# Performance work log

Measured on AMD Instinct MI355X. Metric: run time of the kernel, lower is better.

## Reference

```python
import jax, jax.numpy as jnp
import numpy as np

N_NODES = 100000
N_EDGES = 3200000
IN_CH = 256


def setup_inputs() -> dict:
    key = jax.random.key(0)
    k1, k2, k3 = jax.random.split(key, 3)
    x = jax.random.normal(k1, (N_NODES, IN_CH), dtype=jnp.float32)
    edge_index = jax.random.randint(k2, (2, N_EDGES), 0, N_NODES, dtype=jnp.int64)
    # GCNConv linear: weight [in_channels, 1] (applied as x @ W), bias [1]
    W = jax.random.normal(k3, (IN_CH, 1), dtype=jnp.float32) * (1.0 / np.sqrt(IN_CH))
    b = jnp.zeros((1,), dtype=jnp.float32)
    return {"x": x, "edge_index": edge_index, "W": W, "b": b}


def reference(x, edge_index, W, b):
    # PyG GCNConv(in, 1): h = x @ W; add self-loops; symmetric norm; scatter-add to target; + bias
    N = x.shape[0]
    self_loops = jnp.broadcast_to(jnp.arange(N, dtype=edge_index.dtype)[None, :], (2, N))
    ei = jnp.concatenate([edge_index, self_loops], axis=1)  # [2, E+N]
    src, dst = ei[0], ei[1]

    # degree computed at target (col) with unit edge weights, incl. self-loops
    deg = jax.ops.segment_sum(jnp.ones(ei.shape[1], dtype=x.dtype), dst, num_segments=N)
    deg_inv_sqrt = jnp.where(deg > 0, jax.lax.rsqrt(deg), 0.0)
    norm = deg_inv_sqrt[src] * deg_inv_sqrt[dst]  # [E+N]

    h = x @ W  # [N, 1] — project first (out_channels < in_channels)
    msg = norm[:, None] * h[src]  # [E+N, 1]
    out = jax.ops.segment_sum(msg, dst, num_segments=N)  # [N, 1]
    return out + b
```

## Files before the change

### kernel.cpp

```cpp
#include <hip/hip_runtime.h>

#define GCN_N 100000
#define GCN_E 3200000
#define GCN_C 256
#define BSHIFT 8
#define NBUCK 391
#define BCAP 9216

#define NPROJ 1024
#define NBIN 512
#define TB 512
#define CHUNK (GCN_E / NBIN)
#define EPT ((CHUNK + TB - 1) / TB)

__global__ void k_init(int* __restrict__ cursor) {
    const int i = threadIdx.x;
    if (i < NBUCK) cursor[i] = 0;
}

__global__ void __launch_bounds__(TB) k_proj_bin(const float* __restrict__ x,
                                                 const float* __restrict__ W,
                                                 float* __restrict__ h,
                                                 const int* __restrict__ src,
                                                 const int* __restrict__ dst,
                                                 int* __restrict__ cursor,
                                                 int* __restrict__ bpack) {
    __shared__ int hist[NBUCK];
    __shared__ int lscan[NBUCK];
    __shared__ int gbase[NBUCK];
    __shared__ int wsum[8], woff[8];
    __shared__ int spack[CHUNK];
    __shared__ int sdest[CHUNK];
    const int tid = threadIdx.x;

    if (blockIdx.x < NPROJ) {
        const int lane   = tid & 63;
        const int wave   = (blockIdx.x * TB + tid) >> 6;
        const int nw4    = NPROJ * (TB / 64) * 4;
        const float4 wf = *reinterpret_cast<const float4*>(W + lane * 4);
        for (int i = wave * 4; i < GCN_N; i += nw4) {
            const float4 a0 = *reinterpret_cast<const float4*>(x + (size_t)(i + 0) * GCN_C + lane * 4);
            const float4 a1 = *reinterpret_cast<const float4*>(x + (size_t)(i + 1) * GCN_C + lane * 4);
            const float4 a2 = *reinterpret_cast<const float4*>(x + (size_t)(i + 2) * GCN_C + lane * 4);
            const float4 a3 = *reinterpret_cast<const float4*>(x + (size_t)(i + 3) * GCN_C + lane * 4);
            float s0 = a0.x * wf.x + a0.y * wf.y + a0.z * wf.z + a0.w * wf.w;
            float s1 = a1.x * wf.x + a1.y * wf.y + a1.z * wf.z + a1.w * wf.w;
            float s2 = a2.x * wf.x + a2.y * wf.y + a2.z * wf.z + a2.w * wf.w;
            float s3 = a3.x * wf.x + a3.y * wf.y + a3.z * wf.z + a3.w * wf.w;
            #pragma unroll
            for (int off = 32; off > 0; off >>= 1) {
                s0 += __shfl_down(s0, off, 64);
                s1 += __shfl_down(s1, off, 64);
                s2 += __shfl_down(s2, off, 64);
                s3 += __shfl_down(s3, off, 64);
            }
            if (lane == 0) { h[i] = s0; h[i + 1] = s1; h[i + 2] = s2; h[i + 3] = s3; }
        }
        return;
    }

    const int blk = blockIdx.x - NPROJ;
    for (int b = tid; b < NBUCK; b += TB) hist[b] = 0;
    __syncthreads();

    const int c0 = blk * CHUNK;
    int my_pack[EPT], my_b[EPT], my_off[EPT];
    #pragma unroll
    for (int j = 0; j < EPT; ++j) {
        const int k = tid + j * TB;
        my_b[j] = -1;
        if (k < CHUNK) {
            const int d = dst[c0 + k];
            const int s = src[c0 + k];
            const int b = d >> BSHIFT;
            my_pack[j] = (s << BSHIFT) | (d & 255);
            my_b[j]    = b;
            my_off[j]  = atomicAdd(&hist[b], 1);
        }
    }
    __syncthreads();

    if (tid < NBUCK) gbase[tid] = atomicAdd(&cursor[tid], hist[tid]);
    {
        const int lane = tid & 63, w = tid >> 6;
        const int v = (tid < NBUCK) ? hist[tid] : 0;
        int incl = v;
        #pragma unroll
        for (int d2 = 1; d2 < 64; d2 <<= 1) {
            const int t = __shfl_up(incl, d2, 64);
            if (lane >= d2) incl += t;
        }
        if (lane == 63) wsum[w] = incl;
        __syncthreads();
        if (tid == 0) { int s = 0; for (int k2 = 0; k2 < 8; ++k2) { woff[k2] = s; s += wsum[k2]; } }
        __syncthreads();
        if (tid < NBUCK) lscan[tid] = incl - v + woff[w];
    }
    __syncthreads();

    #pragma unroll
    for (int j = 0; j < EPT; ++j) {
        if (my_b[j] >= 0) {
            const int b    = my_b[j];
            const int slot = lscan[b] + my_off[j];
            const int goff = gbase[b] + my_off[j];
            spack[slot] = my_pack[j];
            sdest[slot] = (goff < BCAP) ? (b * BCAP + goff) : -1;
        }
    }
    __syncthreads();

    for (int i = tid; i < CHUNK; i += TB) {
        const int dpos = sdest[i];
        if (dpos >= 0) bpack[dpos] = spack[i];
    }
}

__global__ void __launch_bounds__(1024) k_deg_norm(const int* __restrict__ bpack,
                                                   const int* __restrict__ cursor,
                                                   const float* __restrict__ h,
                                                   float* __restrict__ dis,
                                                   float* __restrict__ g) {
    __shared__ int cnt[256];
    const int p = blockIdx.x, tid = threadIdx.x;
    if (tid < 256) cnt[tid] = 0;
    __syncthreads();
    const int s0 = p * BCAP, s1 = s0 + min(cursor[p], BCAP);
    for (int i = s0 + tid; i < s1; i += 1024)
        atomicAdd(&cnt[bpack[i] & 255], 1);
    __syncthreads();
    if (tid < 256) {
        const int node = (p << BSHIFT) + tid;
        if (node < GCN_N) {
            const float r = rsqrtf(1.0f + (float)cnt[tid]);
            dis[node] = r;
            g[node]   = r * h[node];
        }
    }
}

__global__ void __launch_bounds__(1024) k_scatter_bin(const int* __restrict__ bpack,
                                                      const int* __restrict__ cursor,
                                                      const float* __restrict__ g,
                                                      const float* __restrict__ dis,
                                                      const float* __restrict__ bias,
                                                      float* __restrict__ out) {
    __shared__ float acc[256];
    const int p = blockIdx.x, tid = threadIdx.x;
    if (tid < 256) acc[tid] = 0.0f;
    __syncthreads();
    const int s0 = p * BCAP, s1 = s0 + min(cursor[p], BCAP);
    for (int i = s0 + tid; i < s1; i += 1024) {
        const int pk = bpack[i];
        atomicAdd(&acc[pk & 255], g[pk >> BSHIFT]);
    }
    __syncthreads();
    if (tid < 256) {
        const int node = (p << BSHIFT) + tid;
        if (node < GCN_N)
            out[node] = bias[0] + dis[node] * (acc[tid] + g[node]);
    }
}

__global__ void k_zero(float* __restrict__ a, int n) {
    int i = blockIdx.x * blockDim.x + threadIdx.x;
    const int stride = gridDim.x * blockDim.x;
    for (; i < n; i += stride) a[i] = 0.0f;
}
__global__ void k_proj_sep(const float* __restrict__ x, const float* __restrict__ W,
                           float* __restrict__ h, int n) {
    const int lane   = threadIdx.x & 63;
    const int wave   = (blockIdx.x * blockDim.x + threadIdx.x) >> 6;
    const int nwaves = (gridDim.x * blockDim.x) >> 6;
    const float4 wf = *reinterpret_cast<const float4*>(W + lane * 4);
    for (int i = wave; i < n; i += nwaves) {
        const float4 xv = *reinterpret_cast<const float4*>(x + (size_t)i * GCN_C + lane * 4);
        float s = xv.x * wf.x + xv.y * wf.y + xv.z * wf.z + xv.w * wf.w;
        #pragma unroll
        for (int off = 32; off > 0; off >>= 1)
            s += __shfl_down(s, off, 64);
        if (lane == 0) h[i] = s;
    }
}
__global__ void k_degree_flat(const int* __restrict__ dst, float* __restrict__ deg, int e) {
    int i = blockIdx.x * blockDim.x + threadIdx.x;
    const int stride = gridDim.x * blockDim.x;
    for (; i < e; i += stride) atomicAdd(&deg[dst[i]], 1.0f);
}
__global__ void k_norm_flat(const float* __restrict__ h, float* __restrict__ deg_dis,
                            float* __restrict__ out, const float* __restrict__ bias, int n) {
    const int i = blockIdx.x * blockDim.x + threadIdx.x;
    if (i < n) {
        const float r = rsqrtf(deg_dis[i] + 1.0f);
        deg_dis[i] = r;
        out[i] = bias[0] + r * r * h[i];
    }
}
__global__ void k_scatter_flat(const int* __restrict__ src, const int* __restrict__ dst,
                               const float* __restrict__ h, const float* __restrict__ dis,
                               float* __restrict__ out, int e) {
    int i = blockIdx.x * blockDim.x + threadIdx.x;
    const int stride = gridDim.x * blockDim.x;
    for (; i < e; i += stride) {
        const int s = src[i], d = dst[i];
        atomicAdd(&out[d], dis[s] * dis[d] * h[s]);
    }
}

extern "C" void kernel_launch(void* const* d_in, const int* in_sizes, int n_in,
                              void* d_out, int out_size, void* d_ws, size_t ws_size,
                              hipStream_t stream) {
    const float* x  = (const float*)d_in[0];
    const int*   ei = (const int*)d_in[1];
    const float* W  = (const float*)d_in[2];
    const float* b  = (const float*)d_in[3];
    float* out = (float*)d_out;
    const int* src = ei;
    const int* dst = ei + GCN_E;

    float* h      = (float*)d_ws;
    float* dis    = h + GCN_N;
    float* g      = dis + GCN_N;
    int*   cursor = (int*)(g + GCN_N);
    int*   bpack  = cursor + NBUCK;
    const size_t need = ((size_t)3 * GCN_N + NBUCK + (size_t)NBUCK * BCAP) * 4;

    if (ws_size >= need) {
        k_init<<<1, TB, 0, stream>>>(cursor);
        k_proj_bin<<<NPROJ + NBIN, TB, 0, stream>>>(x, W, h, src, dst, cursor, bpack);
        k_deg_norm<<<NBUCK, 1024, 0, stream>>>(bpack, cursor, h, dis, g);
        k_scatter_bin<<<NBUCK, 1024, 0, stream>>>(bpack, cursor, g, dis, b, out);
    } else {
        float* hh  = (float*)d_ws;
        float* deg = hh + GCN_N;
        k_zero<<<512, 256, 0, stream>>>(deg, GCN_N);
        k_proj_sep<<<2048, 256, 0, stream>>>(x, W, hh, GCN_N);
        k_degree_flat<<<2048, 256, 0, stream>>>(dst, deg, GCN_E);
        k_norm_flat<<<(GCN_N + 255) / 256, 256, 0, stream>>>(hh, deg, out, b, GCN_N);
        k_scatter_flat<<<2048, 256, 0, stream>>>(src, dst, hh, deg, out, GCN_E);
    }
}
```

Before: 72.18 us.

## Fuse projection into binning blocks instead of separate projection blocks

Removes the dedicated projection blocks and has each of 512 binning blocks (now 1024 threads) also compute the x@W projection for a contiguous slice of rows, placed between the edge histogram and the scan. The aim is to overlap the x stream with the edge binning and drop 1024 extra blocks. In exchange, each block does more serial work, and with fewer total waves the memory parallelism for the 100MB x read may fall. The wave-offset scan loop now runs over only 7 wave sums, which covers the 391 buckets.

```diff
diff --git a/kernel.cpp b/kernel.cpp
--- a/kernel.cpp
+++ b/kernel.cpp
@@ -7,11 +7,11 @@
 #define NBUCK 391
 #define BCAP 9216
 
-#define NPROJ 1024
-#define NBIN 512
-#define TB 512
-#define CHUNK (GCN_E / NBIN)
+#define NBLK 512
+#define TB 1024
+#define CHUNK (GCN_E / NBLK)
 #define EPT ((CHUNK + TB - 1) / TB)
+#define ROWS ((GCN_N + NBLK - 1) / NBLK)
 
 __global__ void k_init(int* __restrict__ cursor) {
     const int i = threadIdx.x;
@@ -28,38 +28,12 @@
     __shared__ int hist[NBUCK];
     __shared__ int lscan[NBUCK];
     __shared__ int gbase[NBUCK];
-    __shared__ int wsum[8], woff[8];
+    __shared__ int wsum[16], woff[16];
     __shared__ int spack[CHUNK];
     __shared__ int sdest[CHUNK];
-    const int tid = threadIdx.x;
-
-    if (blockIdx.x < NPROJ) {
-        const int lane   = tid & 63;
-        const int wave   = (blockIdx.x * TB + tid) >> 6;
-        const int nw4    = NPROJ * (TB / 64) * 4;
-        const float4 wf = *reinterpret_cast<const float4*>(W + lane * 4);
-        for (int i = wave * 4; i < GCN_N; i += nw4) {
-            const float4 a0 = *reinterpret_cast<const float4*>(x + (size_t)(i + 0) * GCN_C + lane * 4);
-            const float4 a1 = *reinterpret_cast<const float4*>(x + (size_t)(i + 1) * GCN_C + lane * 4);
-            const float4 a2 = *reinterpret_cast<const float4*>(x + (size_t)(i + 2) * GCN_C + lane * 4);
-            const float4 a3 = *reinterpret_cast<const float4*>(x + (size_t)(i + 3) * GCN_C + lane * 4);
-            float s0 = a0.x * wf.x + a0.y * wf.y + a0.z * wf.z + a0.w * wf.w;
-            float s1 = a1.x * wf.x + a1.y * wf.y + a1.z * wf.z + a1.w * wf.w;
-            float s2 = a2.x * wf.x + a2.y * wf.y + a2.z * wf.z + a2.w * wf.w;
-            float s3 = a3.x * wf.x + a3.y * wf.y + a3.z * wf.z + a3.w * wf.w;
-            #pragma unroll
-            for (int off = 32; off > 0; off >>= 1) {
-                s0 += __shfl_down(s0, off, 64);
-                s1 += __shfl_down(s1, off, 64);
-                s2 += __shfl_down(s2, off, 64);
-                s3 += __shfl_down(s3, off, 64);
-            }
-            if (lane == 0) { h[i] = s0; h[i + 1] = s1; h[i + 2] = s2; h[i + 3] = s3; }
-        }
-        return;
-    }
-
-    const int blk = blockIdx.x - NPROJ;
+    const int tid = threadIdx.x, blk = blockIdx.x;
+    const int lane = tid & 63, wv = tid >> 6;
+
     for (int b = tid; b < NBUCK; b += TB) hist[b] = 0;
     __syncthreads();
 
@@ -78,11 +52,24 @@
             my_off[j]  = atomicAdd(&hist[b], 1);
         }
     }
+
+    {
+        const float4 wf = *reinterpret_cast<const float4*>(W + lane * 4);
+        const int r0 = blk * ROWS;
+        const int r1 = min(r0 + ROWS, GCN_N);
+        for (int i = r0 + wv; i < r1; i += 16) {
+            const float4 xv = *reinterpret_cast<const float4*>(x + (size_t)i * GCN_C + lane * 4);
+            float s = xv.x * wf.x + xv.y * wf.y + xv.z * wf.z + xv.w * wf.w;
+            #pragma unroll
+            for (int off = 32; off > 0; off >>= 1)
+                s += __shfl_down(s, off, 64);
+            if (lane == 0) h[i] = s;
+        }
+    }
     __syncthreads();
 
     if (tid < NBUCK) gbase[tid] = atomicAdd(&cursor[tid], hist[tid]);
     {
-        const int lane = tid & 63, w = tid >> 6;
         const int v = (tid < NBUCK) ? hist[tid] : 0;
         int incl = v;
         #pragma unroll
@@ -90,11 +77,11 @@
             const int t = __shfl_up(incl, d2, 64);
             if (lane >= d2) incl += t;
         }
-        if (lane == 63) wsum[w] = incl;
+        if (lane == 63) wsum[wv] = incl;
         __syncthreads();
-        if (tid == 0) { int s = 0; for (int k2 = 0; k2 < 8; ++k2) { woff[k2] = s; s += wsum[k2]; } }
+        if (tid == 0) { int s = 0; for (int k2 = 0; k2 < 7; ++k2) { woff[k2] = s; s += wsum[k2]; } }
         __syncthreads();
-        if (tid < NBUCK) lscan[tid] = incl - v + woff[w];
+        if (tid < NBUCK) lscan[tid] = incl - v + woff[wv];
     }
     __syncthreads();
 
@@ -226,8 +213,8 @@
     const size_t need = ((size_t)3 * GCN_N + NBUCK + (size_t)NBUCK * BCAP) * 4;
 
     if (ws_size >= need) {
-        k_init<<<1, TB, 0, stream>>>(cursor);
-        k_proj_bin<<<NPROJ + NBIN, TB, 0, stream>>>(x, W, h, src, dst, cursor, bpack);
+        k_init<<<1, 512, 0, stream>>>(cursor);
+        k_proj_bin<<<NBLK, TB, 0, stream>>>(x, W, h, src, dst, cursor, bpack);
         k_deg_norm<<<NBUCK, 1024, 0, stream>>>(bpack, cursor, h, dis, g);
         k_scatter_bin<<<NBUCK, 1024, 0, stream>>>(bpack, cursor, g, dis, b, out);
     } else {
```

New measurement: 70.55 us. 1.02x faster.
